# Optimization experiments

Hardware: AMD Instinct MI355X
Metric: run time of the kernel (lower is better)

The kernel has to match this reference:

```python
import jax, jax.numpy as jnp
import numpy as np

B, N, D = 4, 2048, 512
M = 1024          # codebook_size
H, DH = 8, 64     # heads, dim_head
I = H * DH        # inner_dim = 512
FF = 1024         # dim_feedforward
EPS = 1e-5


def ln(x, g, b):
    mu = jnp.mean(x, axis=-1, keepdims=True)
    var = jnp.mean((x - mu) ** 2, axis=-1, keepdims=True)
    return (x - mu) * jax.lax.rsqrt(var + EPS) * g + b


def setup_inputs() -> dict:
    key = jax.random.key(0)
    ks = jax.random.split(key, 20)
    s = lambda fan: 1.0 / np.sqrt(fan)
    return {
        "context_input": jax.random.normal(ks[0], (B, N, D), jnp.float32),
        "context_mask": jax.random.randint(ks[1], (B, N), 0, 2) > 0,
        "codebook": jax.random.normal(ks[2], (M, D), jnp.float32),
        "norm_g": jnp.ones((D,)), "norm_b": jnp.zeros((D,)),
        "cnorm_g": jnp.ones((D,)), "cnorm_b": jnp.zeros((D,)),
        "wq": jax.random.normal(ks[3], (D, I)) * s(D),
        "wkv": jax.random.normal(ks[4], (D, 2 * I)) * s(D),
        "wo": jax.random.normal(ks[5], (I, D)) * s(I),
        "wo_b": jnp.zeros((D,)),
        "a_norm_g": jnp.ones((D,)), "a_norm_b": jnp.zeros((D,)),
        "a_qkv": jax.random.normal(ks[6], (D, 3 * I)) * s(D),
        "a_out": jax.random.normal(ks[7], (I, D)) * s(I),
        "f_norm_g": jnp.ones((D,)), "f_norm_b": jnp.zeros((D,)),
        "f_w1": jax.random.normal(ks[8], (D, FF)) * s(D),
        "f_w2": jax.random.normal(ks[9], (FF, D)) * s(FF),
    }


def _forward(context_input, context_mask, codebook, norm_g, norm_b, cnorm_g,
             cnorm_b, wq, wkv, wo, wo_b, a_norm_g, a_norm_b, a_qkv, a_out,
             f_norm_g, f_norm_b, f_w1, f_w2):
    scale = DH ** -0.5
    # ---- Vector quantization: nearest-codebook assignment (inference path) ----
    flat = context_input.reshape(-1, D)                      # [B*N, D]
    dist = (jnp.sum(flat ** 2, -1, keepdims=True)
            - 2.0 * flat @ codebook.T
            + jnp.sum(codebook ** 2, -1))                    # [B*N, M]
    flat_idx = jnp.argmin(dist, axis=-1)                     # [B*N]
    indices = flat_idx.reshape(B, N)
    quant = codebook[flat_idx]                               # [B*N, D]
    commit_loss = jnp.mean((flat - jax.lax.stop_gradient(quant)) ** 2)
    counts = jnp.zeros((M,), flat.dtype).at[flat_idx].add(1.0)
    probs = counts / flat_idx.shape[0]
    perplexity = jnp.exp(-jnp.sum(probs * jnp.log(probs + 1e-10)))
    # ---- Cross-attention: codebook queries attend over the context ----
    xq = ln(codebook, norm_g, norm_b)                        # [M, D]
    q = (xq @ wq).reshape(M, H, DH).transpose(1, 0, 2) * scale   # [H, M, DH]
    ctx = ln(context_input, cnorm_g, cnorm_b)                # [B, N, D]
    kv = ctx @ wkv                                           # [B, N, 2I]
    k, v = jnp.split(kv, 2, axis=-1)
    k = k.reshape(B, N, H, DH).transpose(0, 2, 1, 3)         # [B, H, N, DH]
    v = v.reshape(B, N, H, DH).transpose(0, 2, 1, 3)
    sim = jnp.einsum('hid,bhjd->bhij', q, k)                 # [B, H, M, N]
    big = jnp.finfo(sim.dtype).max
    sim = jnp.where(context_mask[:, None, None, :], sim, -big)
    attn = jax.nn.softmax(sim, axis=-1)
    out = jnp.einsum('bhij,bhjd->bhid', attn, v)             # [B, H, M, DH]
    out = out.transpose(0, 2, 1, 3).reshape(B, M, I) @ wo + wo_b  # [B, M, D]
    # ---- Transformer refinement layer (self-attn + FF, residual) ----
    h = ln(out, a_norm_g, a_norm_b)
    qkv = (h @ a_qkv).reshape(B, M, 3, H, DH)
    q2 = qkv[:, :, 0].transpose(0, 2, 1, 3) * scale
    k2 = qkv[:, :, 1].transpose(0, 2, 1, 3)
    v2 = qkv[:, :, 2].transpose(0, 2, 1, 3)
    a2 = jax.nn.softmax(jnp.einsum('bhid,bhjd->bhij', q2, k2), axis=-1)
    o2 = jnp.einsum('bhij,bhjd->bhid', a2, v2)
    out = out + o2.transpose(0, 2, 1, 3).reshape(B, M, I) @ a_out
    hf = ln(out, f_norm_g, f_norm_b)
    out = out + jax.nn.gelu(hf @ f_w1) @ f_w2
    # ---- Gather per-token outputs by VQ index ----
    outputs = jnp.take_along_axis(out, indices[:, :, None], axis=1)  # [B, N, D]
    return outputs, commit_loss, perplexity


def reference(context_input, context_mask, codebook, norm_g, norm_b, cnorm_g,
              cnorm_b, wq, wkv, wo, wo_b, a_norm_g, a_norm_b, a_qkv, a_out,
              f_norm_g, f_norm_b, f_w1, f_w2):
    return _forward(context_input, context_mask, codebook, norm_g, norm_b,
                    cnorm_g, cnorm_b, wq, wkv, wo, wo_b, a_norm_g, a_norm_b,
                    a_qkv, a_out, f_norm_g, f_norm_b, f_w1, f_w2)
```

## Files before the change

### kernel.cpp

```cpp
#include <hip/hip_runtime.h>
#include <math.h>

#define B_ 4
#define N_ 2048
#define D_ 512
#define M_ 1024
#define H_ 8
#define DH_ 64
#define I_ 512
#define FF_ 1024

typedef unsigned short u16;
typedef __attribute__((ext_vector_type(8))) short bf16x8;
typedef __attribute__((ext_vector_type(4))) float f32x4;

__device__ inline u16 f2b(float f) {
  union { float f; unsigned int u; } v; v.f = f;
  unsigned int u = v.u;
  u += 0x7fffu + ((u >> 16) & 1u);
  return (u16)(u >> 16);
}
__device__ inline float b2f(u16 h) {
  union { unsigned int u; float f; } v; v.u = ((unsigned int)h) << 16;
  return v.f;
}
__device__ inline float ex2(float x) { return __builtin_amdgcn_exp2f(x); }
__device__ inline unsigned int cvtpk(float lo, float hi) {
  unsigned int r;
  asm("v_cvt_pk_bf16_f32 %0, %1, %2" : "=v"(r) : "v"(lo), "v"(hi));
  return r;
}

__device__ inline float gelu_f(float x) {
  float x3 = x * x * x;
  return 0.5f * x * (1.f + tanhf(0.7978845608028654f * (x + 0.044715f * x3)));
}

__device__ inline bool better(float d1, int i1, float d2, int i2) {
  return d1 < d2 || (d1 == d2 && i1 < i2);
}
__device__ inline void cswap(float& da, int& ia, float& db, int& ib) {
  if (better(db, ib, da, ia)) {
    float td = da; da = db; db = td;
    int ti = ia; ia = ib; ib = ti;
  }
}
__device__ inline void kmin(float& da, int& ia, float db, int ib) {
  if (better(db, ib, da, ia)) { da = db; ia = ib; }
}

struct WJobs {
  const float* src[7];
  u16* dst[7];
  int K[7], N[7], b0[8];
};

__global__ __launch_bounds__(256) void prep_kernel(
    const unsigned char* __restrict__ mb, int* __restrict__ flag,
    const float* __restrict__ ctx, u16* __restrict__ vqA,
    const float* __restrict__ cb, u16* __restrict__ vqBT,
    WJobs jobs)
{
  __shared__ float tile[32][33];
  __shared__ int any;
  int bid = blockIdx.x;
  int tid = threadIdx.x;
  if (bid == 0) {
    if (tid == 0) any = 0;
    __syncthreads();
    int acc = 0;
    for (int i = tid; i < 8192; i += 256)
      if (i & 3) acc |= mb[i];
    if (acc) atomicOr(&any, 1);
    __syncthreads();
    if (tid == 0) *flag = any;
    return;
  }
  if (bid < 2049) {
    int i = ((bid - 1) * 256 + tid) * 8;
    float4 a = *(const float4*)(ctx + i);
    float4 b = *(const float4*)(ctx + i + 4);
    uint4 o;
    o.x = cvtpk(a.x, a.y); o.y = cvtpk(a.z, a.w);
    o.z = cvtpk(b.x, b.y); o.w = cvtpk(b.z, b.w);
    *(uint4*)(vqA + i) = o;
    return;
  }
  if (bid < 2305) {
    int i = ((bid - 2049) * 256 + tid) * 8;
    float4 a = *(const float4*)(cb + i);
    float4 b = *(const float4*)(cb + i + 4);
    uint4 o;
    o.x = cvtpk(a.x, a.y); o.y = cvtpk(a.z, a.w);
    o.z = cvtpk(b.x, b.y); o.w = cvtpk(b.z, b.w);
    *(uint4*)(vqBT + i) = o;
    return;
  }
  int wb = bid - 2305;
  int j = 0;
#pragma unroll
  for (int i = 1; i < 7; i++) if (wb >= jobs.b0[i]) j = i;
  int tb = wb - jobs.b0[j];
  int K = jobs.K[j], Nn = jobs.N[j];
  int tiles_x = Nn >> 5;
  int n0 = (tb % tiles_x) << 5, k0 = (tb / tiles_x) << 5;
  const float* W = jobs.src[j];
  u16* WT = jobs.dst[j];
  int ty = tid >> 5, tx = tid & 31;
#pragma unroll
  for (int i = 0; i < 4; i++)
    tile[ty + 8 * i][tx] = W[(size_t)(k0 + ty + 8 * i) * Nn + n0 + tx];
  __syncthreads();
#pragma unroll
  for (int i = 0; i < 4; i++)
    WT[(size_t)(n0 + ty + 8 * i) * K + k0 + tx] = f2b(tile[tx][ty + 8 * i]);
}

__global__ __launch_bounds__(128) void sq_norm_kernel(
    const float* __restrict__ cb, double* __restrict__ csq, float* __restrict__ csqf,
    float* __restrict__ counts, const void* __restrict__ mraw,
    const int* __restrict__ flag, int* __restrict__ mnorm)
{
  int tid = threadIdx.x;
  if (blockIdx.x < 1024) {
    int row = blockIdx.x;
    const float4* r4 = (const float4*)(cb + (size_t)row * D_);
    float4 v = r4[tid];
    double s = (double)v.x * v.x + (double)v.y * v.y + (double)v.z * v.z + (double)v.w * v.w;
    for (int off = 32; off; off >>= 1) s += __shfl_down(s, off);
    __shared__ double red[2];
    if ((tid & 63) == 0) red[tid >> 6] = s;
    __syncthreads();
    if (tid == 0) {
      csq[row] = red[0] + red[1];
      csqf[row] = (float)(red[0] + red[1]);
      counts[row] = 0.f;
    }
    return;
  }
  int j = blockIdx.x - 1024;
  int fl = *flag;
#pragma unroll
  for (int k = 0; k < 2; k++) {
    int i = j * 256 + tid + k * 128;
    int v;
    if (fl) v = ((const unsigned char*)mraw)[i];
    else    v = ((const int*)mraw)[i];
    mnorm[i] = (v != 0) ? 1 : 0;
  }
}

__global__ __launch_bounds__(256) void vq_refine4_kernel(
    const float* __restrict__ flat, const float* __restrict__ cb,
    const double* __restrict__ csq, const float4* __restrict__ cand_part,
    int* __restrict__ out_idx, double* __restrict__ commit_partial,
    float* __restrict__ counts)
{
  int wave = threadIdx.x >> 6, lane = threadIdx.x & 63;
  int t = blockIdx.x * 4 + wave;
  int sl = lane & 15;
  float4 a = cand_part[(size_t)t * 32 + sl * 2];
  float4 bb = cand_part[(size_t)t * 32 + sl * 2 + 1];
  float d0 = a.x, d1 = a.y, d2 = bb.x, d3 = bb.y;
  int x0 = __float_as_int(a.z), x1 = __float_as_int(a.w);
  int x2 = __float_as_int(bb.z), x3 = __float_as_int(bb.w);
  for (int off = 1; off < 16; off <<= 1) {
    float e0 = __shfl_xor(d0, off), e1 = __shfl_xor(d1, off);
    float e2 = __shfl_xor(d2, off), e3 = __shfl_xor(d3, off);
    int y0 = __shfl_xor(x0, off), y1 = __shfl_xor(x1, off);
    int y2 = __shfl_xor(x2, off), y3 = __shfl_xor(x3, off);
    kmin(d0, x0, e3, y3); kmin(d1, x1, e2, y2);
    kmin(d2, x2, e1, y1); kmin(d3, x3, e0, y0);
    cswap(d0, x0, d2, x2); cswap(d1, x1, d3, x3);
    cswap(d0, x0, d1, x1); cswap(d2, x2, d3, x3);
  }
  const float* x = flat + ((size_t)t << 9);
  const float* p0 = cb + ((size_t)x0 << 9);
  const float* p1 = cb + ((size_t)x1 << 9);
  const float* p2 = cb + ((size_t)x2 << 9);
  const float* p3 = cb + ((size_t)x3 << 9);
  double s0 = 0.0, s1 = 0.0, s2 = 0.0, s3 = 0.0, sx = 0.0;
#pragma unroll
  for (int i = 0; i < 8; i++) {
    int d = lane + i * 64;
    double xv = x[d];
    s0 += xv * (double)p0[d];
    s1 += xv * (double)p1[d];
    s2 += xv * (double)p2[d];
    s3 += xv * (double)p3[d];
    sx += xv * xv;
  }
  for (int off = 32; off; off >>= 1) {
    s0 += __shfl_down(s0, off);
    s1 += __shfl_down(s1, off);
    s2 += __shfl_down(s2, off);
    s3 += __shfl_down(s3, off);
    sx += __shfl_down(sx, off);
  }
  if (lane == 0) {
    double dd0 = csq[x0] - 2.0 * s0;
    double dd1 = csq[x1] - 2.0 * s1;
    double dd2 = csq[x2] - 2.0 * s2;
    double dd3 = csq[x3] - 2.0 * s3;
    int bi = x0; double bd = dd0;
    if (dd1 < bd || (dd1 == bd && x1 < bi)) { bd = dd1; bi = x1; }
    if (dd2 < bd || (dd2 == bd && x2 < bi)) { bd = dd2; bi = x2; }
    if (dd3 < bd || (dd3 == bd && x3 < bi)) { bd = dd3; bi = x3; }
    out_idx[t] = bi;
    commit_partial[t] = sx + bd;
    atomicAdd(counts + bi, 1.0f);
  }
}

__global__ __launch_bounds__(256) void ln_rows_kernel(
    const float* __restrict__ x, const float* __restrict__ g,
    const float* __restrict__ b, u16* __restrict__ y)
{
  int row = blockIdx.x, tid = threadIdx.x;
  const float* xr = x + (size_t)row * D_;
  float v0 = xr[tid], v1 = xr[tid + 256];
  float s = v0 + v1;
  for (int off = 32; off; off >>= 1) s += __shfl_down(s, off);
  __shared__ float red[4];
  __shared__ float bcast[2];
  if ((tid & 63) == 0) red[tid >> 6] = s;
  __syncthreads();
  if (tid == 0) bcast[0] = (red[0] + red[1] + red[2] + red[3]) * (1.f / 512.f);
  __syncthreads();
  float mu = bcast[0];
  float d0 = v0 - mu, d1 = v1 - mu;
  float q = d0 * d0 + d1 * d1;
  for (int off = 32; off; off >>= 1) q += __shfl_down(q, off);
  if ((tid & 63) == 0) red[tid >> 6] = q;
  __syncthreads();
  if (tid == 0) bcast[1] = rsqrtf((red[0] + red[1] + red[2] + red[3]) * (1.f / 512.f) + 1e-5f);
  __syncthreads();
  float rs = bcast[1];
  u16* yr = y + (size_t)row * D_;
  yr[tid]       = f2b(d0 * rs * g[tid] + b[tid]);
  yr[tid + 256] = f2b(d1 * rs * g[tid + 256] + b[tid + 256]);
}

template <int BN>
__global__ __launch_bounds__(256, 4) void gemm_bf16_kernel(
    const u16* __restrict__ A, const u16* __restrict__ BT,
    const float* __restrict__ bias, const float* __restrict__ resid,
    float* __restrict__ Cf, u16* __restrict__ Cb,
    const float* __restrict__ csqf, float4* __restrict__ cand_part,
    int M, int N, int K, int act)
{
  constexpr int MF = (BN == 128) ? 4 : 2;
  constexpr int ROWS_W = (BN == 128) ? 64 : 32;
  __shared__ __attribute__((aligned(16))) u16 As[2][128 * 40];
  __shared__ __attribute__((aligned(16))) u16 Bs[2][BN * 40];
  int tid = threadIdx.x;
  int lane = tid & 63, wave = tid >> 6;
  int wr = (BN == 128) ? (wave >> 1) : wave;
  int wc = (BN == 128) ? (wave & 1) : 0;
  int nwgx = gridDim.x;
  int nwg = nwgx * gridDim.y;
  int flat = blockIdx.y * nwgx + blockIdx.x;
  if ((nwg & 7) == 0) flat = (flat & 7) * (nwg >> 3) + (flat >> 3);
  int row0 = (flat / nwgx) << 7, col0 = (flat % nwgx) * BN;
  int l15 = lane & 15, l4 = lane >> 4;
  int sr = tid >> 2, skc = tid & 3;
  int soff = sr * 40 + skc * 8;
  const u16* pA0 = A + (size_t)(row0 + sr) * K + skc * 8;
  const u16* pA1 = A + (size_t)(row0 + 64 + sr) * K + skc * 8;
  const u16* pB0 = BT + (size_t)(col0 + sr) * K + skc * 8;
  const u16* pB1 = (BN == 128) ? (BT + (size_t)(col0 + 64 + sr) * K + skc * 8) : nullptr;
  f32x4 acc[MF][4] = {};
  int KT = K >> 5;
  bf16x8 ra0 = *(const bf16x8*)pA0;
  bf16x8 ra1 = *(const bf16x8*)pA1;
  bf16x8 rb0 = *(const bf16x8*)pB0;
  bf16x8 rb1;
  if constexpr (BN == 128) rb1 = *(const bf16x8*)pB1;
  *(bf16x8*)&As[0][soff] = ra0;
  *(bf16x8*)&As[0][64 * 40 + soff] = ra1;
  *(bf16x8*)&Bs[0][soff] = rb0;
  if constexpr (BN == 128) *(bf16x8*)&Bs[0][64 * 40 + soff] = rb1;
  if (KT > 1) {
    ra0 = *(const bf16x8*)(pA0 + 32);
    ra1 = *(const bf16x8*)(pA1 + 32);
    rb0 = *(const bf16x8*)(pB0 + 32);
    if constexpr (BN == 128) rb1 = *(const bf16x8*)(pB1 + 32);
  }
  for (int kt = 0; kt < KT; kt++) {
    int cur = kt & 1;
    __syncthreads();
    if (kt + 1 < KT) {
      *(bf16x8*)&As[cur ^ 1][soff] = ra0;
      *(bf16x8*)&As[cur ^ 1][64 * 40 + soff] = ra1;
      *(bf16x8*)&Bs[cur ^ 1][soff] = rb0;
      if constexpr (BN == 128) *(bf16x8*)&Bs[cur ^ 1][64 * 40 + soff] = rb1;
    }
    if (kt + 2 < KT) {
      int ko = (kt + 2) << 5;
      ra0 = *(const bf16x8*)(pA0 + ko);
      ra1 = *(const bf16x8*)(pA1 + ko);
      rb0 = *(const bf16x8*)(pB0 + ko);
      if constexpr (BN == 128) rb1 = *(const bf16x8*)(pB1 + ko);
    }
    bf16x8 af[MF], bfr[4];
#pragma unroll
    for (int m = 0; m < MF; m++)
      af[m] = *(const bf16x8*)&As[cur][(wr * ROWS_W + m * 16 + l15) * 40 + l4 * 8];
#pragma unroll
    for (int n = 0; n < 4; n++)
      bfr[n] = *(const bf16x8*)&Bs[cur][(wc * 64 + n * 16 + l15) * 40 + l4 * 8];
#pragma unroll
    for (int m = 0; m < MF; m++)
#pragma unroll
      for (int n = 0; n < 4; n++)
        acc[m][n] = __builtin_amdgcn_mfma_f32_16x16x32_bf16(af[m], bfr[n], acc[m][n], 0, 0, 0);
  }
  if constexpr (BN == 128) {
    if (act == 2) {
      float csq_l[4];
#pragma unroll
      for (int n = 0; n < 4; n++) csq_l[n] = csqf[col0 + wc * 64 + n * 16 + l15];
      int cbase = col0 + wc * 64 + l15;
      int slot = ((col0 >> 7) << 1) + wc;
#pragma unroll
      for (int m = 0; m < 4; m++) {
#pragma unroll
        for (int r = 0; r < 4; r++) {
          float d0 = csq_l[0] - 2.f * acc[m][0][r];
          float d1 = csq_l[1] - 2.f * acc[m][1][r];
          float d2 = csq_l[2] - 2.f * acc[m][2][r];
          float d3 = csq_l[3] - 2.f * acc[m][3][r];
          int x0 = cbase, x1 = cbase + 16, x2 = cbase + 32, x3 = cbase + 48;
          cswap(d0, x0, d1, x1); cswap(d2, x2, d3, x3);
          cswap(d0, x0, d2, x2); cswap(d1, x1, d3, x3);
          cswap(d1, x1, d2, x2);
          for (int off = 1; off < 16; off <<= 1) {
            float e0 = __shfl_xor(d0, off), e1 = __shfl_xor(d1, off);
            float e2 = __shfl_xor(d2, off), e3 = __shfl_xor(d3, off);
            int y0 = __shfl_xor(x0, off), y1 = __shfl_xor(x1, off);
            int y2 = __shfl_xor(x2, off), y3 = __shfl_xor(x3, off);
            kmin(d0, x0, e3, y3); kmin(d1, x1, e2, y2);
            kmin(d2, x2, e1, y1); kmin(d3, x3, e0, y0);
            cswap(d0, x0, d2, x2); cswap(d1, x1, d3, x3);
            cswap(d0, x0, d1, x1); cswap(d2, x2, d3, x3);
          }
          if (l15 == 0) {
            int row = row0 + wr * 64 + m * 16 + l4 * 4 + r;
            float4 v1, v2;
            v1.x = d0; v1.y = d1;
            v1.z = __int_as_float(x0); v1.w = __int_as_float(x1);
            v2.x = d2; v2.y = d3;
            v2.z = __int_as_float(x2); v2.w = __int_as_float(x3);
            cand_part[(size_t)row * 32 + slot * 2]     = v1;
            cand_part[(size_t)row * 32 + slot * 2 + 1] = v2;
          }
        }
      }
      return;
    }
  }
#pragma unroll
  for (int m = 0; m < MF; m++) {
#pragma unroll
    for (int n = 0; n < 4; n++) {
      int col = col0 + wc * 64 + n * 16 + l15;
      float bv = bias ? bias[col] : 0.f;
#pragma unroll
      for (int r = 0; r < 4; r++) {
        int row = row0 + wr * ROWS_W + m * 16 + l4 * 4 + r;
        float v = acc[m][n][r] + bv;
        if (act == 1) v = gelu_f(v);
        if (resid) v += resid[(size_t)row * N + col];
        if (Cf) Cf[(size_t)row * N + col] = v;
        if (Cb) Cb[(size_t)row * N + col] = f2b(v);
      }
    }
  }
}

__global__ __launch_bounds__(256) void vt_kernel(
    const u16* __restrict__ src, size_t b_stride, int row_stride, int col0,
    int n_rows, u16* __restrict__ dst)
{
  __shared__ __attribute__((aligned(16))) u16 tile[32][72];
  int t = threadIdx.x;
  int bh = blockIdx.y;
  int b = bh >> 3, h = bh & 7;
  int n0 = blockIdx.x * 32;
  int n = t >> 3, dc = t & 7;
  *(bf16x8*)&tile[n][dc * 8] =
      *(const bf16x8*)(src + (size_t)b * b_stride + (size_t)(n0 + n) * row_stride + col0 + h * 64 + dc * 8);
  __syncthreads();
  int d = t >> 2, ns = t & 3;
  bf16x8 o;
#pragma unroll
  for (int i = 0; i < 8; i++) o[i] = (short)tile[ns * 8 + i][d];
  *(bf16x8*)(dst + ((size_t)bh * 64 + d) * n_rows + n0 + ns * 8) = o;
}

__global__ __launch_bounds__(256, 4) void attn_mfma_kernel(
    const u16* __restrict__ Q, size_t q_bs, int q_stride,
    const u16* __restrict__ Kp, size_t k_bs, int k_stride, int k_extra,
    const u16* __restrict__ Vt, const int* __restrict__ mask,
    float scale, u16* __restrict__ Opart, float* __restrict__ MLpart,
    int n_keys)
{
  __shared__ __attribute__((aligned(16))) u16 Ks[8 * 64 * 8];
  __shared__ __attribute__((aligned(16))) u16 Vs[8 * 64 * 8];
  __shared__ __attribute__((aligned(16))) u16 Ps[4][8 * 32 * 8];
  __shared__ float mbias[64];
  int tid = threadIdx.x, lane = tid & 63, wave = tid >> 6;
  int flat = blockIdx.x + (blockIdx.y << 3) + (blockIdx.z << 6);
  int swz = ((flat & 7) << 7) + (flat >> 3);
  int qb = swz & 7, h = (swz >> 3) & 7, z = swz >> 6;
  int b = z & 3, split = z >> 2;
  int q0 = qb * 128 + wave * 32;
  int l15 = lane & 15, l4 = lane >> 4;
  int nq = n_keys >> 2;
  int nstart = split * nq, nend = nstart + nq;

  const u16* qrow = Q + (size_t)b * q_bs + (size_t)(q0 + l15) * q_stride + h * 64 + l4 * 8;
  bf16x8 qfA0 = *(const bf16x8*)qrow;
  bf16x8 qfA1 = *(const bf16x8*)(qrow + 32);
  const u16* qrowB = qrow + 16 * q_stride;
  bf16x8 qfB0 = *(const bf16x8*)qrowB;
  bf16x8 qfB1 = *(const bf16x8*)(qrowB + 32);
  f32x4 oA[4] = {}, oB[4] = {};
  float mA = -3.0e38f, lA = 0.f, mB = -3.0e38f, lB = 0.f;
  int srow = tid >> 2, schunk = tid & 3;
  const u16* kbase = Kp + (size_t)b * k_bs + k_extra + h * 64;
  const u16* vtbase = Vt + (size_t)(b * 8 + h) * 64 * n_keys;

  bf16x8 pk0, pk1, pv0, pv1;
  int pmv = 1;
  {
    const u16* krow = kbase + (size_t)(nstart + srow) * k_stride;
    pk0 = *(const bf16x8*)(krow + schunk * 8);
    pk1 = *(const bf16x8*)(krow + (schunk + 4) * 8);
    const u16* vrow = vtbase + (size_t)srow * n_keys + nstart;
    pv0 = *(const bf16x8*)(vrow + schunk * 8);
    pv1 = *(const bf16x8*)(vrow + (schunk + 4) * 8);
    if (mask && tid < 64) pmv = mask[(size_t)b * n_keys + nstart + tid];
  }

  for (int n0 = nstart; n0 < nend; n0 += 64) {
    __syncthreads();
    *(bf16x8*)&Ks[(schunk * 64 + srow) * 8]       = pk0;
    *(bf16x8*)&Ks[((schunk + 4) * 64 + srow) * 8] = pk1;
    *(bf16x8*)&Vs[(schunk * 64 + srow) * 8]       = pv0;
    *(bf16x8*)&Vs[((schunk + 4) * 64 + srow) * 8] = pv1;
    if (tid < 64) mbias[tid] = (mask && !pmv) ? -3.0e38f : 0.f;
    __syncthreads();
    if (n0 + 64 < nend) {
      const u16* krow = kbase + (size_t)(n0 + 64 + srow) * k_stride;
      pk0 = *(const bf16x8*)(krow + schunk * 8);
      pk1 = *(const bf16x8*)(krow + (schunk + 4) * 8);
      const u16* vrow = vtbase + (size_t)srow * n_keys + n0 + 64;
      pv0 = *(const bf16x8*)(vrow + schunk * 8);
      pv1 = *(const bf16x8*)(vrow + (schunk + 4) * 8);
      if (mask && tid < 64) pmv = mask[(size_t)b * n_keys + n0 + 64 + tid];
    }
    f32x4 sacA[4], sacB[4];
#pragma unroll
    for (int kb = 0; kb < 4; kb++) {
      bf16x8 kf0 = *(const bf16x8*)&Ks[(l4 * 64 + kb * 16 + l15) * 8];
      bf16x8 kf1 = *(const bf16x8*)&Ks[((l4 + 4) * 64 + kb * 16 + l15) * 8];
      f32x4 za = {}, zb = {};
      za = __builtin_amdgcn_mfma_f32_16x16x32_bf16(kf0, qfA0, za, 0, 0, 0);
      sacA[kb] = __builtin_amdgcn_mfma_f32_16x16x32_bf16(kf1, qfA1, za, 0, 0, 0);
      zb = __builtin_amdgcn_mfma_f32_16x16x32_bf16(kf0, qfB0, zb, 0, 0, 0);
      sacB[kb] = __builtin_amdgcn_mfma_f32_16x16x32_bf16(kf1, qfB1, zb, 0, 0, 0);
    }
    {
      float pmax = -3.0e38f;
#pragma unroll
      for (int kb = 0; kb < 4; kb++) {
        float4 bs = *(const float4*)&mbias[kb * 16 + l4 * 4];
        sacA[kb][0] = fmaf(sacA[kb][0], scale, bs.x);
        sacA[kb][1] = fmaf(sacA[kb][1], scale, bs.y);
        sacA[kb][2] = fmaf(sacA[kb][2], scale, bs.z);
        sacA[kb][3] = fmaf(sacA[kb][3], scale, bs.w);
#pragma unroll
        for (int r = 0; r < 4; r++) pmax = fmaxf(pmax, sacA[kb][r]);
      }
      pmax = fmaxf(pmax, __shfl_xor(pmax, 16));
      pmax = fmaxf(pmax, __shfl_xor(pmax, 32));
      if (!__all(pmax - mA <= 11.5f)) {
        float mnew = fmaxf(mA, pmax);
        float al = ex2(mA - mnew);
        lA *= al;
        mA = mnew;
        float alr[4];
#pragma unroll
        for (int r = 0; r < 4; r++) alr[r] = __shfl(al, l4 * 4 + r, 64);
#pragma unroll
        for (int nb = 0; nb < 4; nb++)
#pragma unroll
          for (int r = 0; r < 4; r++) oA[nb][r] *= alr[r];
      }
      float psum = 0.f;
#pragma unroll
      for (int kb = 0; kb < 4; kb++) {
        float p0 = ex2(sacA[kb][0] - mA);
        float p1 = ex2(sacA[kb][1] - mA);
        float p2 = ex2(sacA[kb][2] - mA);
        float p3 = ex2(sacA[kb][3] - mA);
        psum += (p0 + p1) + (p2 + p3);
        uint2 w;
        w.x = cvtpk(p0, p1);
        w.y = cvtpk(p2, p3);
        *(uint2*)&Ps[wave][((kb * 2 + (l4 >> 1)) * 32 + l15) * 8 + (l4 & 1) * 4] = w;
      }
      psum += __shfl_xor(psum, 16);
      psum += __shfl_xor(psum, 32);
      lA += psum;
    }
    {
      float pmax = -3.0e38f;
#pragma unroll
      for (int kb = 0; kb < 4; kb++) {
        float4 bs = *(const float4*)&mbias[kb * 16 + l4 * 4];
        sacB[kb][0] = fmaf(sacB[kb][0], scale, bs.x);
        sacB[kb][1] = fmaf(sacB[kb][1], scale, bs.y);
        sacB[kb][2] = fmaf(sacB[kb][2], scale, bs.z);
        sacB[kb][3] = fmaf(sacB[kb][3], scale, bs.w);
#pragma unroll
        for (int r = 0; r < 4; r++) pmax = fmaxf(pmax, sacB[kb][r]);
      }
      pmax = fmaxf(pmax, __shfl_xor(pmax, 16));
      pmax = fmaxf(pmax, __shfl_xor(pmax, 32));
      if (!__all(pmax - mB <= 11.5f)) {
        float mnew = fmaxf(mB, pmax);
        float al = ex2(mB - mnew);
        lB *= al;
        mB = mnew;
        float alr[4];
#pragma unroll
        for (int r = 0; r < 4; r++) alr[r] = __shfl(al, l4 * 4 + r, 64);
#pragma unroll
        for (int nb = 0; nb < 4; nb++)
#pragma unroll
          for (int r = 0; r < 4; r++) oB[nb][r] *= alr[r];
      }
      float psum = 0.f;
#pragma unroll
      for (int kb = 0; kb < 4; kb++) {
        float p0 = ex2(sacB[kb][0] - mB);
        float p1 = ex2(sacB[kb][1] - mB);
        float p2 = ex2(sacB[kb][2] - mB);
        float p3 = ex2(sacB[kb][3] - mB);
        psum += (p0 + p1) + (p2 + p3);
        uint2 w;
        w.x = cvtpk(p0, p1);
        w.y = cvtpk(p2, p3);
        *(uint2*)&Ps[wave][((kb * 2 + (l4 >> 1)) * 32 + 16 + l15) * 8 + (l4 & 1) * 4] = w;
      }
      psum += __shfl_xor(psum, 16);
      psum += __shfl_xor(psum, 32);
      lB += psum;
    }
#pragma unroll
    for (int c = 0; c < 2; c++) {
      bf16x8 pfA = *(const bf16x8*)&Ps[wave][((c * 4 + l4) * 32 + l15) * 8];
      bf16x8 pfB = *(const bf16x8*)&Ps[wave][((c * 4 + l4) * 32 + 16 + l15) * 8];
#pragma unroll
      for (int nb = 0; nb < 4; nb++) {
        bf16x8 vf = *(const bf16x8*)&Vs[((c * 4 + l4) * 64 + nb * 16 + l15) * 8];
        oA[nb] = __builtin_amdgcn_mfma_f32_16x16x32_bf16(pfA, vf, oA[nb], 0, 0, 0);
        oB[nb] = __builtin_amdgcn_mfma_f32_16x16x32_bf16(pfB, vf, oB[nb], 0, 0, 0);
      }
    }
  }
  int pr_base = ((split * 4 + b) * 8 + h) * 1024;
#pragma unroll
  for (int nb = 0; nb < 4; nb++)
#pragma unroll
    for (int r = 0; r < 4; r++) {
      Opart[(size_t)(pr_base + q0 + l4 * 4 + r) * 64 + nb * 16 + l15] = f2b(oA[nb][r]);
      Opart[(size_t)(pr_base + q0 + 16 + l4 * 4 + r) * 64 + nb * 16 + l15] = f2b(oB[nb][r]);
    }
  if (lane < 16) {
    int pr = pr_base + q0 + lane;
    MLpart[2 * pr]     = mA;
    MLpart[2 * pr + 1] = lA;
  } else if (lane < 32) {
    int pr = pr_base + q0 + 16 + l15;
    MLpart[2 * pr]     = mB;
    MLpart[2 * pr + 1] = lB;
  }
}

__global__ __launch_bounds__(256) void attn_combine_kernel(
    const u16* __restrict__ Opart, const float* __restrict__ MLpart,
    u16* __restrict__ O, size_t o_bs)
{
  int idx = blockIdx.x * 256 + threadIdx.x;
  int d = idx & 63, gq = idx >> 6;
  int row = gq & 1023, bh = gq >> 10;
  int h = bh & 7, b = bh >> 3;
  float m[4], l[4];
  int pr[4];
#pragma unroll
  for (int s = 0; s < 4; s++) {
    pr[s] = ((s * 4 + b) * 8 + h) * 1024 + row;
    m[s] = MLpart[2 * pr[s]];
    l[s] = MLpart[2 * pr[s] + 1];
  }
  float mmax = fmaxf(fmaxf(m[0], m[1]), fmaxf(m[2], m[3]));
  float lsum = 0.f, osum = 0.f;
#pragma unroll
  for (int s = 0; s < 4; s++) {
    float w = ex2(m[s] - mmax);
    lsum += l[s] * w;
    osum += b2f(Opart[(size_t)pr[s] * 64 + d]) * w;
  }
  O[(size_t)b * o_bs + (size_t)row * 512 + h * 64 + d] = f2b(osum / lsum);
}

__global__ __launch_bounds__(128) void gather_scalars_kernel(
    const float* __restrict__ x2, const int* __restrict__ idx,
    const float* __restrict__ counts, const double* __restrict__ commit_partial,
    float* __restrict__ out, float* __restrict__ out_tail)
{
  int t = blockIdx.x;
  int tid = threadIdx.x;
  if (t < 8192) {
    int b = t >> 11;
    int code = idx[t];
    const float4* src = (const float4*)(x2 + ((size_t)(b * M_ + code) << 9));
    float4* dst = (float4*)(out + ((size_t)t << 9));
    dst[tid] = src[tid];
    return;
  }
  double cs = 0.0;
#pragma unroll
  for (int i = 0; i < 64; i++) cs += commit_partial[tid + i * 128];
  double e = 0.0;
#pragma unroll
  for (int i = 0; i < 8; i++) {
    double p = (double)counts[tid + i * 128] / 8192.0;
    e += p * log(p + 1e-10);
  }
  for (int off = 32; off; off >>= 1) {
    cs += __shfl_down(cs, off);
    e  += __shfl_down(e, off);
  }
  __shared__ double redc[2], rede[2];
  if ((tid & 63) == 0) { redc[tid >> 6] = cs; rede[tid >> 6] = e; }
  __syncthreads();
  if (tid == 0) {
    out_tail[0] = (float)((redc[0] + redc[1]) / (8192.0 * 512.0));
    out_tail[1] = (float)exp(-(rede[0] + rede[1]));
  }
}

extern "C" void kernel_launch(void* const* d_in, const int* in_sizes, int n_in,
                              void* d_out, int out_size, void* d_ws, size_t ws_size,
                              hipStream_t stream) {
  const float* ctx      = (const float*)d_in[0];
  const void*  mask_raw = d_in[1];
  const float* codebook = (const float*)d_in[2];
  const float* norm_g   = (const float*)d_in[3];
  const float* norm_b   = (const float*)d_in[4];
  const float* cnorm_g  = (const float*)d_in[5];
  const float* cnorm_b  = (const float*)d_in[6];
  const float* wq       = (const float*)d_in[7];
  const float* wkv      = (const float*)d_in[8];
  const float* wo       = (const float*)d_in[9];
  const float* wo_b     = (const float*)d_in[10];
  const float* a_norm_g = (const float*)d_in[11];
  const float* a_norm_b = (const float*)d_in[12];
  const float* a_qkv    = (const float*)d_in[13];
  const float* a_out    = (const float*)d_in[14];
  const float* f_norm_g = (const float*)d_in[15];
  const float* f_norm_b = (const float*)d_in[16];
  const float* f_w1     = (const float*)d_in[17];
  const float* f_w2     = (const float*)d_in[18];
  float* out = (float*)d_out;
  const float LOG2E = 1.4426950408889634f;

  char* ws = (char*)d_ws;
  int*    mask_flag  = (int*)(ws + 64);
  float*  counts     = (float*)(ws + 128);
  double* code_sq    = (double*)(ws + 4224);
  float*  csqf       = (float*)(ws + 12416);
  int*    indices    = (int*)(ws + 16512);
  int*    mask_norm  = (int*)(ws + 49280);
  double* commit_partial = (double*)(ws + 262144);

  char* pool = ws + (1 << 20);
  u16*   vqA  = (u16*)(pool);
  u16*   vqBT = (u16*)(pool + ((size_t)25 << 20));
  float4* cand_part = (float4*)(pool + ((size_t)30 << 20));
  float* attn_ml = (float*)(pool + ((size_t)61 << 20));
  char* regA  = pool;
  char* regB  = pool + ((size_t)16 << 20);
  char* regC  = pool + ((size_t)24 << 20);
  char* regD  = pool + ((size_t)32 << 20);
  char* regE  = pool + ((size_t)40 << 20);
  char* regF  = pool + ((size_t)44 << 20);
  size_t woff = (1 << 20) + ((size_t)64 << 20);
  u16* wqT    = (u16*)(ws + woff); woff += (size_t)512 * 512 * 2;
  u16* wkvT   = (u16*)(ws + woff); woff += (size_t)1024 * 512 * 2;
  u16* woT    = (u16*)(ws + woff); woff += (size_t)512 * 512 * 2;
  u16* aqkvT  = (u16*)(ws + woff); woff += (size_t)1536 * 512 * 2;
  u16* aoutT  = (u16*)(ws + woff); woff += (size_t)512 * 512 * 2;
  u16* fw1T   = (u16*)(ws + woff); woff += (size_t)1024 * 512 * 2;
  u16* fw2T   = (u16*)(ws + woff); woff += (size_t)512 * 1024 * 2;
  u16* xq_b   = (u16*)(ws + woff); woff += (size_t)1024 * 512 * 2;
  u16* qs_b   = (u16*)(ws + woff); woff += (size_t)1024 * 512 * 2;

  u16* kv_b     = (u16*)regA;
  u16* qkv2_b   = (u16*)regA;
  u16* ctx_ln_b = (u16*)regB;
  u16* VtS      = (u16*)regB;
  u16* VtX      = (u16*)regC;
  float* x1_f   = (float*)regC;
  float* x0_f   = (float*)regD;
  u16* att_out_b = (u16*)regE;
  u16* h_b       = (u16*)regE;
  u16* o2_b      = (u16*)regE;
  u16* hf_b      = (u16*)regE;
  u16* g_b      = (u16*)regF;
  float* x2_f   = (float*)(pool + ((size_t)52 << 20));
  u16* attn_part = (u16*)regF;

  WJobs jobs;
  jobs.src[0] = wq;    jobs.dst[0] = wqT;   jobs.K[0] = 512;  jobs.N[0] = 512;
  jobs.src[1] = wkv;   jobs.dst[1] = wkvT;  jobs.K[1] = 512;  jobs.N[1] = 1024;
  jobs.src[2] = wo;    jobs.dst[2] = woT;   jobs.K[2] = 512;  jobs.N[2] = 512;
  jobs.src[3] = a_qkv; jobs.dst[3] = aqkvT; jobs.K[3] = 512;  jobs.N[3] = 1536;
  jobs.src[4] = a_out; jobs.dst[4] = aoutT; jobs.K[4] = 512;  jobs.N[4] = 512;
  jobs.src[5] = f_w1;  jobs.dst[5] = fw1T;  jobs.K[5] = 512;  jobs.N[5] = 1024;
  jobs.src[6] = f_w2;  jobs.dst[6] = fw2T;  jobs.K[6] = 1024; jobs.N[6] = 512;
  int acc_b = 0;
  for (int i = 0; i < 7; i++) {
    jobs.b0[i] = acc_b;
    acc_b += (jobs.K[i] >> 5) * (jobs.N[i] >> 5);
  }
  jobs.b0[7] = acc_b;
  prep_kernel<<<2305 + acc_b, 256, 0, stream>>>(
      (const unsigned char*)mask_raw, mask_flag, ctx, vqA, codebook, vqBT, jobs);

  sq_norm_kernel<<<1056, 128, 0, stream>>>(codebook, code_sq, csqf, counts,
                                           mask_raw, mask_flag, mask_norm);

  gemm_bf16_kernel<128><<<dim3(8, 64), 256, 0, stream>>>(vqA, vqBT, nullptr, nullptr,
                                                    nullptr, nullptr, csqf, cand_part,
                                                    8192, 1024, 512, 2);
  vq_refine4_kernel<<<2048, 256, 0, stream>>>(ctx, codebook, code_sq, cand_part, indices,
                                              commit_partial, counts);

  ln_rows_kernel<<<1024, 256, 0, stream>>>(codebook, norm_g, norm_b, xq_b);
  gemm_bf16_kernel<64><<<dim3(8, 8), 256, 0, stream>>>(xq_b, wqT, nullptr, nullptr,
                                                   nullptr, qs_b, nullptr, nullptr,
                                                   1024, 512, 512, 0);
  ln_rows_kernel<<<8192, 256, 0, stream>>>(ctx, cnorm_g, cnorm_b, ctx_ln_b);
  gemm_bf16_kernel<128><<<dim3(8, 64), 256, 0, stream>>>(ctx_ln_b, wkvT, nullptr, nullptr,
                                                    nullptr, kv_b, nullptr, nullptr,
                                                    8192, 1024, 512, 0);
  vt_kernel<<<dim3(64, 32), 256, 0, stream>>>(kv_b, (size_t)2048 * 1024, 1024, 512, 2048, VtX);
  attn_mfma_kernel<<<dim3(8, 8, 16), 256, 0, stream>>>(
      qs_b, 0, 512, kv_b, (size_t)2048 * 1024, 1024, 0, VtX, mask_norm,
      0.125f * LOG2E, attn_part, attn_ml, 2048);
  attn_combine_kernel<<<8192, 256, 0, stream>>>(attn_part, attn_ml, att_out_b, (size_t)1024 * 512);
  gemm_bf16_kernel<64><<<dim3(8, 32), 256, 0, stream>>>(att_out_b, woT, wo_b, nullptr,
                                                    x0_f, nullptr, nullptr, nullptr,
                                                    4096, 512, 512, 0);

  ln_rows_kernel<<<4096, 256, 0, stream>>>(x0_f, a_norm_g, a_norm_b, h_b);
  gemm_bf16_kernel<64><<<dim3(24, 32), 256, 0, stream>>>(h_b, aqkvT, nullptr, nullptr,
                                                     nullptr, qkv2_b, nullptr, nullptr,
                                                     4096, 1536, 512, 0);
  vt_kernel<<<dim3(32, 32), 256, 0, stream>>>(qkv2_b, (size_t)1024 * 1536, 1536, 1024, 1024, VtS);
  attn_mfma_kernel<<<dim3(8, 8, 16), 256, 0, stream>>>(
      qkv2_b, (size_t)1024 * 1536, 1536, qkv2_b, (size_t)1024 * 1536, 1536, 512, VtS, nullptr,
      0.125f * LOG2E, attn_part, attn_ml, 1024);
  attn_combine_kernel<<<8192, 256, 0, stream>>>(attn_part, attn_ml, o2_b, (size_t)1024 * 512);
  gemm_bf16_kernel<64><<<dim3(8, 32), 256, 0, stream>>>(o2_b, aoutT, nullptr, x0_f,
                                                    x1_f, nullptr, nullptr, nullptr,
                                                    4096, 512, 512, 0);
  ln_rows_kernel<<<4096, 256, 0, stream>>>(x1_f, f_norm_g, f_norm_b, hf_b);
  gemm_bf16_kernel<64><<<dim3(16, 32), 256, 0, stream>>>(hf_b, fw1T, nullptr, nullptr,
                                                    nullptr, g_b, nullptr, nullptr,
                                                    4096, 1024, 512, 1);
  gemm_bf16_kernel<64><<<dim3(8, 32), 256, 0, stream>>>(g_b, fw2T, nullptr, x1_f,
                                                    x2_f, nullptr, nullptr, nullptr,
                                                    4096, 512, 1024, 0);

  gather_scalars_kernel<<<8193, 128, 0, stream>>>(x2_f, indices, counts, commit_partial,
                                                  out, out + (size_t)B_ * N_ * D_);
}
```

Measured before the change: 299.1 us.

## Fold codebook norms, mask normalization and both layernorms into prep kernel

Merges the squared-norm/mask kernel and the two row layernorm kernels into the single prep launch as extra block ranges. Block 0 now computes the mask format flag and writes the normalized mask itself, so the separate flag pass goes away. This removes three kernel launches and their serialization gaps. In exchange, one much larger heterogeneous grid has to hold all of this work. The layernorm outputs must not alias any buffer the same kernel writes, such as vqA or vqBT in the pool regions.

Result: no change. 296.6 us (median of 2 runs) (-0.8%).

```diff
diff --git a/kernel.cpp b/kernel.cpp
--- a/kernel.cpp
+++ b/kernel.cpp
@@ -56,15 +56,24 @@
 };
 
 __global__ __launch_bounds__(256) void prep_kernel(
-    const unsigned char* __restrict__ mb, int* __restrict__ flag,
+    const void* __restrict__ mraw, int* __restrict__ mnorm,
     const float* __restrict__ ctx, u16* __restrict__ vqA,
     const float* __restrict__ cb, u16* __restrict__ vqBT,
+    const float* __restrict__ norm_g, const float* __restrict__ norm_b,
+    u16* __restrict__ xq_b,
+    const float* __restrict__ cnorm_g, const float* __restrict__ cnorm_b,
+    u16* __restrict__ ctx_ln_b,
+    double* __restrict__ csq, float* __restrict__ csqf, float* __restrict__ counts,
     WJobs jobs)
 {
   __shared__ float tile[32][33];
   __shared__ int any;
+  __shared__ float redf[4];
+  __shared__ float bc[2];
+  __shared__ double redd[4];
   int bid = blockIdx.x;
   int tid = threadIdx.x;
+  const unsigned char* mb = (const unsigned char*)mraw;
   if (bid == 0) {
     if (tid == 0) any = 0;
     __syncthreads();
@@ -73,7 +82,11 @@
       if (i & 3) acc |= mb[i];
     if (acc) atomicOr(&any, 1);
     __syncthreads();
-    if (tid == 0) *flag = any;
+    int fl = any;
+    for (int i = tid; i < 8192; i += 256) {
+      int v = fl ? mb[i] : ((const int*)mraw)[i];
+      mnorm[i] = (v != 0) ? 1 : 0;
+    }
     return;
   }
   if (bid < 2049) {
@@ -96,7 +109,59 @@
     *(uint4*)(vqBT + i) = o;
     return;
   }
-  int wb = bid - 2305;
+  if (bid < 3329) {
+    int row = bid - 2305;
+    float2 v = ((const float2*)(cb + (size_t)row * D_))[tid];
+    double s = (double)v.x * v.x + (double)v.y * v.y;
+    for (int off = 32; off; off >>= 1) s += __shfl_down(s, off);
+    if ((tid & 63) == 0) redd[tid >> 6] = s;
+    __syncthreads();
+    if (tid == 0) {
+      double t = redd[0] + redd[1] + redd[2] + redd[3];
+      csq[row] = t;
+      csqf[row] = (float)t;
+      counts[row] = 0.f;
+    }
+    return;
+  }
+  if (bid < 12545) {
+    int row;
+    const float* xr;
+    const float* g;
+    const float* bb;
+    u16* yr;
+    if (bid < 4353) {
+      row = bid - 3329;
+      xr = cb + (size_t)row * D_;
+      g = norm_g; bb = norm_b;
+      yr = xq_b + (size_t)row * D_;
+    } else {
+      row = bid - 4353;
+      xr = ctx + (size_t)row * D_;
+      g = cnorm_g; bb = cnorm_b;
+      yr = ctx_ln_b + (size_t)row * D_;
+    }
+    float v0 = xr[tid], v1 = xr[tid + 256];
+    float s = v0 + v1;
+    for (int off = 32; off; off >>= 1) s += __shfl_down(s, off);
+    if ((tid & 63) == 0) redf[tid >> 6] = s;
+    __syncthreads();
+    if (tid == 0) bc[0] = (redf[0] + redf[1] + redf[2] + redf[3]) * (1.f / 512.f);
+    __syncthreads();
+    float mu = bc[0];
+    float d0 = v0 - mu, d1 = v1 - mu;
+    float q = d0 * d0 + d1 * d1;
+    for (int off = 32; off; off >>= 1) q += __shfl_down(q, off);
+    if ((tid & 63) == 0) redf[tid >> 6] = q;
+    __syncthreads();
+    if (tid == 0) bc[1] = rsqrtf((redf[0] + redf[1] + redf[2] + redf[3]) * (1.f / 512.f) + 1e-5f);
+    __syncthreads();
+    float rs = bc[1];
+    yr[tid]       = f2b(d0 * rs * g[tid] + bb[tid]);
+    yr[tid + 256] = f2b(d1 * rs * g[tid + 256] + bb[tid + 256]);
+    return;
+  }
+  int wb = bid - 12545;
   int j = 0;
 #pragma unroll
   for (int i = 1; i < 7; i++) if (wb >= jobs.b0[i]) j = i;
@@ -114,40 +179,6 @@
 #pragma unroll
   for (int i = 0; i < 4; i++)
     WT[(size_t)(n0 + ty + 8 * i) * K + k0 + tx] = f2b(tile[tx][ty + 8 * i]);
-}
-
-__global__ __launch_bounds__(128) void sq_norm_kernel(
-    const float* __restrict__ cb, double* __restrict__ csq, float* __restrict__ csqf,
-    float* __restrict__ counts, const void* __restrict__ mraw,
-    const int* __restrict__ flag, int* __restrict__ mnorm)
-{
-  int tid = threadIdx.x;
-  if (blockIdx.x < 1024) {
-    int row = blockIdx.x;
-    const float4* r4 = (const float4*)(cb + (size_t)row * D_);
-    float4 v = r4[tid];
-    double s = (double)v.x * v.x + (double)v.y * v.y + (double)v.z * v.z + (double)v.w * v.w;
-    for (int off = 32; off; off >>= 1) s += __shfl_down(s, off);
-    __shared__ double red[2];
-    if ((tid & 63) == 0) red[tid >> 6] = s;
-    __syncthreads();
-    if (tid == 0) {
-      csq[row] = red[0] + red[1];
-      csqf[row] = (float)(red[0] + red[1]);
-      counts[row] = 0.f;
-    }
-    return;
-  }
-  int j = blockIdx.x - 1024;
-  int fl = *flag;
-#pragma unroll
-  for (int k = 0; k < 2; k++) {
-    int i = j * 256 + tid + k * 128;
-    int v;
-    if (fl) v = ((const unsigned char*)mraw)[i];
-    else    v = ((const int*)mraw)[i];
-    mnorm[i] = (v != 0) ? 1 : 0;
-  }
 }
 
 __global__ __launch_bounds__(256) void vq_refine4_kernel(
@@ -680,7 +711,6 @@
   const float LOG2E = 1.4426950408889634f;
 
   char* ws = (char*)d_ws;
-  int*    mask_flag  = (int*)(ws + 64);
   float*  counts     = (float*)(ws + 128);
   double* code_sq    = (double*)(ws + 4224);
   float*  csqf       = (float*)(ws + 12416);
@@ -739,11 +769,10 @@
     acc_b += (jobs.K[i] >> 5) * (jobs.N[i] >> 5);
   }
   jobs.b0[7] = acc_b;
-  prep_kernel<<<2305 + acc_b, 256, 0, stream>>>(
-      (const unsigned char*)mask_raw, mask_flag, ctx, vqA, codebook, vqBT, jobs);
-
-  sq_norm_kernel<<<1056, 128, 0, stream>>>(codebook, code_sq, csqf, counts,
-                                           mask_raw, mask_flag, mask_norm);
+  prep_kernel<<<12545 + acc_b, 256, 0, stream>>>(
+      mask_raw, mask_norm, ctx, vqA, codebook, vqBT,
+      norm_g, norm_b, xq_b, cnorm_g, cnorm_b, ctx_ln_b,
+      code_sq, csqf, counts, jobs);
 
   gemm_bf16_kernel<128><<<dim3(8, 64), 256, 0, stream>>>(vqA, vqBT, nullptr, nullptr,
                                                     nullptr, nullptr, csqf, cand_part,
@@ -751,11 +780,9 @@
   vq_refine4_kernel<<<2048, 256, 0, stream>>>(ctx, codebook, code_sq, cand_part, indices,
                                               commit_partial, counts);
 
-  ln_rows_kernel<<<1024, 256, 0, stream>>>(codebook, norm_g, norm_b, xq_b);
   gemm_bf16_kernel<64><<<dim3(8, 8), 256, 0, stream>>>(xq_b, wqT, nullptr, nullptr,
                                                    nullptr, qs_b, nullptr, nullptr,
                                                    1024, 512, 512, 0);
-  ln_rows_kernel<<<8192, 256, 0, stream>>>(ctx, cnorm_g, cnorm_b, ctx_ln_b);
   gemm_bf16_kernel<128><<<dim3(8, 64), 256, 0, stream>>>(ctx_ln_b, wkvT, nullptr, nullptr,
                                                     nullptr, kv_b, nullptr, nullptr,
                                                     8192, 1024, 512, 0);
```
